# Kernel tuning notes

Measured on AMD Instinct MI355X. Metric: run time of the kernel, lower is better.

Reference implementation:

```python
import jax, jax.numpy as jnp
import numpy as np

UNITS = 256
LB = -17.0
UB = 8.0
STEP = 0.05
NUM_BUCKETS = int((UB - LB) / STEP) + 1  # 501
RESIDUE = LB - STEP
W_INIT = 0.5
BATCH = 65536


def setup_inputs() -> dict:
    key = jax.random.key(0)
    kx, = jax.random.split(key, 1)
    x = jax.random.normal(kx, (BATCH, UNITS), dtype=jnp.float32)
    v = jnp.ones((UNITS, NUM_BUCKETS), dtype=jnp.float32) * W_INIT
    b = jnp.zeros((UNITS,), dtype=jnp.float32)
    return {"x": x, "v": v, "b": b}


def reference(x, v, b):
    # x: (batch, units); v: (units, num_buckets); b: (units,)
    x_clipped = jnp.clip(x, LB + 1e-9, UB - 1e-9)
    indx = ((x_clipped - LB + STEP) / STEP).astype(jnp.int32)
    indx = jnp.clip(indx, 0, NUM_BUCKETS - 1)  # (batch, units)
    delta = x_clipped - LB + STEP - indx.astype(x.dtype) * STEP

    w = jax.nn.relu(v)  # (units, num_buckets)
    # exclusive cumsum over buckets: csum[u, j] = sum_{k<j} w[u, k]
    csum = jnp.cumsum(w, axis=1)
    csum = jnp.concatenate([jnp.zeros((w.shape[0], 1), w.dtype), csum[:, :-1]], axis=1)

    unit_idx = jnp.arange(UNITS)[None, :]  # (1, units) broadcasts with indx
    csum_g = csum[unit_idx, indx]  # (batch, units)
    w_g = w[unit_idx, indx]        # (batch, units)

    # Equivalent to sum over buckets of (triangular step mask + scattered delta) * relu(v)
    logits = STEP * csum_g + delta * w_g + RESIDUE + b[None, :]
    return jax.nn.sigmoid(logits)
```

## Files before the change

kernel.cpp:

```cpp
#include <hip/hip_runtime.h>

#define UNITS 256
#define NB 501
#define STEPF 0.05f
#define LBF -17.0f
#define UBF 8.0f
#define RESIDUEF -17.05f
#define LOG2E 1.4426950408889634f

#define WLO 192
#define WSZ 256
#define UPB 16
#define PADF2 257
#define THREADS 512
#define ROWS_PB 1024

__global__ __launch_bounds__(256) void build_table_kernel(
    const float* __restrict__ v, const float* __restrict__ b,
    float2* __restrict__ gtab) {
  const int lane = threadIdx.x & 63;
  const int wave = threadIdx.x >> 6;
  const int u = blockIdx.x * 4 + wave;
  if (u >= UNITS) return;

  const float* vu = v + u * NB;
  float w[8], pref[8];
  float run = 0.0f;
#pragma unroll
  for (int k = 0; k < 8; ++k) {
    const int j = lane * 8 + k;
    const float wv = (j < NB) ? fmaxf(vu[j], 0.0f) : 0.0f;
    w[k] = wv;
    pref[k] = run;
    run += wv;
  }
  float s = run;
#pragma unroll
  for (int d = 1; d < 64; d <<= 1) {
    const float o = __shfl_up(s, d, 64);
    if (lane >= d) s += o;
  }
  const float base = s - run;
  const float off = RESIDUEF + b[u];
#pragma unroll
  for (int k = 0; k < 8; ++k) {
    const int j = lane * 8 + k;
    if (j < NB) {
      const float C = STEPF * (base + pref[k]) + off - (float)j * STEPF * w[k];
      gtab[u * NB + j] = make_float2(C * LOG2E, w[k] * LOG2E);
    }
  }
}

__global__ __launch_bounds__(THREADS, 8) void iso_main_kernel(
    const float* __restrict__ x, const float2* __restrict__ gtab,
    float* __restrict__ out) {
  __shared__ float2 tab[UPB * PADF2];

  const int bu = blockIdx.x & (UNITS / UPB - 1);
  const int bb = blockIdx.x >> 4;
  const int u0 = bu * UPB;

  for (int i = threadIdx.x; i < UPB * WSZ; i += THREADS) {
    const int ul = i >> 8;
    const int j = i & (WSZ - 1);
    tab[ul * PADF2 + j] = gtab[(u0 + ul) * NB + WLO + j];
  }

  const int r = threadIdx.x >> 2;
  const int q = threadIdx.x & 3;
  const float4* __restrict__ x4 = reinterpret_cast<const float4*>(x);
  float4* __restrict__ o4 = reinterpret_cast<float4*>(out);
  const int g0 = (bb * ROWS_PB + r) * (UNITS / 4) + (u0 >> 2) + q;

  float4 xv[8];
#pragma unroll
  for (int p = 0; p < 8; ++p) xv[p] = x4[g0 + p * 128 * (UNITS / 4)];

  __syncthreads();

  const int qbase = (4 * q) * PADF2;
#pragma unroll
  for (int p = 0; p < 8; ++p) {
    const float xs[4] = {xv[p].x, xv[p].y, xv[p].z, xv[p].w};
    float os[4];
#pragma unroll
    for (int k = 0; k < 4; ++k) {
      const float xc = fminf(fmaxf(xs[k], LBF + 1e-9f), UBF - 1e-9f);
      const float t = xc - LBF + STEPF;
      int idx = (int)(t * 20.0f);
      const unsigned iw = (unsigned)(idx - WLO);
      float2 cw;
      if (iw < WSZ) {
        cw = tab[qbase + k * PADF2 + (int)iw];
      } else {
        idx = idx < 0 ? 0 : (idx > NB - 1 ? NB - 1 : idx);
        cw = gtab[(u0 + 4 * q + k) * NB + idx];
      }
      const float l2 = fmaf(t, cw.y, cw.x);
      const float e = __builtin_amdgcn_exp2f(-l2);
      os[k] = __builtin_amdgcn_rcpf(1.0f + e);
    }
    o4[g0 + p * 128 * (UNITS / 4)] = make_float4(os[0], os[1], os[2], os[3]);
  }
}

extern "C" void kernel_launch(void* const* d_in, const int* in_sizes, int n_in,
                              void* d_out, int out_size, void* d_ws,
                              size_t ws_size, hipStream_t stream) {
  const float* x = (const float*)d_in[0];
  const float* v = (const float*)d_in[1];
  const float* b = (const float*)d_in[2];
  float* out = (float*)d_out;
  float2* gtab = (float2*)d_ws;

  build_table_kernel<<<64, 256, 0, stream>>>(v, b, gtab);

  const int rows = out_size / UNITS;
  const int grid = (UNITS / UPB) * (rows / ROWS_PB);
  iso_main_kernel<<<grid, THREADS, 0, stream>>>(x, gtab, out);
}
```

Baseline: 144.2 us.

## Widen unit tile to 64 per block and software-pipeline row loads

```diff
diff --git a/kernel.cpp b/kernel.cpp
--- a/kernel.cpp
+++ b/kernel.cpp
@@ -10,10 +10,12 @@
 
 #define WLO 192
 #define WSZ 256
-#define UPB 16
+#define UPB 64
 #define PADF2 257
-#define THREADS 512
+#define THREADS 1024
 #define ROWS_PB 1024
+#define CHUNKS 16
+#define RDEPTH 4
 
 __global__ __launch_bounds__(256) void build_table_kernel(
     const float* __restrict__ v, const float* __restrict__ b,
@@ -52,37 +54,44 @@
   }
 }
 
-__global__ __launch_bounds__(THREADS, 8) void iso_main_kernel(
+__global__ __launch_bounds__(THREADS, 4) void iso_main_kernel(
     const float* __restrict__ x, const float2* __restrict__ gtab,
     float* __restrict__ out) {
   __shared__ float2 tab[UPB * PADF2];
 
-  const int bu = blockIdx.x & (UNITS / UPB - 1);
-  const int bb = blockIdx.x >> 4;
+  const int bu = blockIdx.x & 3;
+  const int bb = blockIdx.x >> 2;
   const int u0 = bu * UPB;
 
+#pragma unroll
   for (int i = threadIdx.x; i < UPB * WSZ; i += THREADS) {
     const int ul = i >> 8;
     const int j = i & (WSZ - 1);
     tab[ul * PADF2 + j] = gtab[(u0 + ul) * NB + WLO + j];
   }
+  __syncthreads();
 
-  const int r = threadIdx.x >> 2;
-  const int q = threadIdx.x & 3;
+  const int lane = threadIdx.x & 63;
+  const int wv = threadIdx.x >> 6;
+  const int rowoff = wv * 4 + (lane >> 4);
+  const int col4 = lane & 15;
   const float4* __restrict__ x4 = reinterpret_cast<const float4*>(x);
   float4* __restrict__ o4 = reinterpret_cast<float4*>(out);
-  const int g0 = (bb * ROWS_PB + r) * (UNITS / 4) + (u0 >> 2) + q;
+  const int g0 = (bb * ROWS_PB + rowoff) * (UNITS / 4) + bu * 16 + col4;
+  const int gstep = 64 * (UNITS / 4);
+  const int qbase = (col4 * 4) * PADF2;
 
-  float4 xv[8];
+  float4 xv[RDEPTH];
 #pragma unroll
-  for (int p = 0; p < 8; ++p) xv[p] = x4[g0 + p * 128 * (UNITS / 4)];
+  for (int c = 0; c < RDEPTH; ++c) xv[c] = x4[g0 + c * gstep];
 
-  __syncthreads();
+#pragma unroll
+  for (int c = 0; c < CHUNKS; ++c) {
+    const float4 cur = xv[c & (RDEPTH - 1)];
+    if (c + RDEPTH < CHUNKS)
+      xv[c & (RDEPTH - 1)] = x4[g0 + (c + RDEPTH) * gstep];
 
-  const int qbase = (4 * q) * PADF2;
-#pragma unroll
-  for (int p = 0; p < 8; ++p) {
-    const float xs[4] = {xv[p].x, xv[p].y, xv[p].z, xv[p].w};
+    const float xs[4] = {cur.x, cur.y, cur.z, cur.w};
     float os[4];
 #pragma unroll
     for (int k = 0; k < 4; ++k) {
@@ -95,13 +104,13 @@
         cw = tab[qbase + k * PADF2 + (int)iw];
       } else {
         idx = idx < 0 ? 0 : (idx > NB - 1 ? NB - 1 : idx);
-        cw = gtab[(u0 + 4 * q + k) * NB + idx];
+        cw = gtab[(u0 + col4 * 4 + k) * NB + idx];
       }
       const float l2 = fmaf(t, cw.y, cw.x);
       const float e = __builtin_amdgcn_exp2f(-l2);
       os[k] = __builtin_amdgcn_rcpf(1.0f + e);
     }
-    o4[g0 + p * 128 * (UNITS / 4)] = make_float4(os[0], os[1], os[2], os[3]);
+    o4[g0 + c * gstep] = make_float4(os[0], os[1], os[2], os[3]);
   }
 }
 
```

After: 133.8 us. 7.2% less time.
